# Optimization experiments

Hardware: AMD Instinct MI355X
Metric: run time of the kernel (lower is better)

## Reference

```python
import jax, jax.numpy as jnp
import numpy as np
from jax import lax

B, DIM, H, DM, NH = 32, 16, 128, 256, 8  # batch, in-channels, seq, d_model, n_head


def setup_inputs() -> dict:
    key = jax.random.key(0)
    k1, k2, k3, k4, k5 = jax.random.split(key, 5)
    x = jax.random.normal(k1, (B, DIM, H, DM), jnp.float32)
    conv1_w = jax.random.normal(k2, (3 * NH * DIM, 1, 5, 1), jnp.float32) * 0.1
    conv2_w = jax.random.normal(k3, (3 * NH * DIM, 1, 1, NH), jnp.float32) * 0.1
    w_out_w = jax.random.normal(k4, (DM, DM), jnp.float32) * (1.0 / np.sqrt(DM))
    w_out_b = jax.random.normal(k5, (DM,), jnp.float32) * 0.01
    return dict(x=x, conv1_w=conv1_w, conv2_w=conv2_w, w_out_w=w_out_w, w_out_b=w_out_b)


def reference(x, conv1_w, conv2_w, w_out_w, w_out_b):
    b, dim, h, w = x.shape
    nh = conv2_w.shape[-1]
    dn = ('NCHW', 'OIHW', 'NCHW')
    # grouped conv (5,1), padding 'same' on height, groups=dim
    y = lax.conv_general_dilated(x, conv1_w, (1, 1), [(2, 2), (0, 0)],
                                 dimension_numbers=dn, feature_group_count=dim)
    # depthwise conv (1, nh) stride (1, nh): width w -> w/nh
    y = lax.conv_general_dilated(y, conv2_w, (1, nh), [(0, 0), (0, 0)],
                                 dimension_numbers=dn, feature_group_count=y.shape[1])
    # dropout layers are identity in eval mode
    C = nh * dim
    wp = w // nh
    y = y.reshape(b, 3, C, h, wp)  # 'b (n c) h w -> n b c h w' split, n=3 outer
    q, k, v = y[:, 0], y[:, 1], y[:, 2]  # each [b, C, h, wp]
    scores = jnp.einsum('bcqd,bckd->bcqk', q, k) / jnp.sqrt(jnp.float32(wp))
    attn = jax.nn.softmax(scores, axis=-1)
    o = jnp.einsum('bcqk,bckd->bcqd', attn, v)  # [b, C, h, wp]
    # 'b (c n) h w -> b c h (n w)' with c=dim, n=nh
    o = o.reshape(b, dim, nh, h, wp).transpose(0, 1, 3, 2, 4).reshape(b, dim, h, nh * wp)
    return o @ w_out_w.T + w_out_b
```

## Files before the change

kernel.cpp:

```cpp
#include <hip/hip_runtime.h>
#include <stdint.h>

#define B_   32
#define DIM_ 16
#define H_   128
#define DM_  256
#define NH_  8
#define WP_  32
#define C3_  384

typedef short bf16x8 __attribute__((ext_vector_type(8)));
typedef float f32x4  __attribute__((ext_vector_type(4)));

__device__ __forceinline__ unsigned short f2bfu(float v) {
    unsigned int x = __float_as_uint(v);
    x += 0x7fffu + ((x >> 16) & 1u);
    return (unsigned short)(x >> 16);
}
__device__ __forceinline__ unsigned cvtpk(float lo, float hi) {
    unsigned r;
    asm("v_cvt_pk_bf16_f32 %0, %1, %2" : "=v"(r) : "v"(lo), "v"(hi));
    return r;
}
__device__ __forceinline__ void gl_lds16(const void* g, void* l) {
    __builtin_amdgcn_global_load_lds(
        (const __attribute__((address_space(1))) unsigned int*)g,
        (__attribute__((address_space(3))) unsigned int*)l, 16, 0, 0);
}

__global__ __launch_bounds__(256) void conv_kernel(
    const float* __restrict__ x, const float* __restrict__ w1,
    const float* __restrict__ w2, unsigned short* __restrict__ y2)
{
    __shared__ float wlds[24 * 16];

    const int bid = blockIdx.x;
    const int ht = bid & 1;
    const int g  = (bid >> 1) & 15;
    const int b  = bid >> 5;
    const int tid = threadIdx.x;
    const int wp = tid & 31;
    const int hl = tid >> 5;
    const int h0 = ht * 64 + hl * 8;

    for (int i = tid; i < 384; i += 256) {
        const int oc = i >> 4, ix = i & 15;
        const int o = g * 24 + oc;
        float v = 0.f;
        if (ix < 5)       v = w1[o * 5 + ix];
        else if (ix < 13) v = w2[o * 8 + (ix - 5)];
        wlds[i] = v;
    }

    const float* xbase = x + ((size_t)(b * DIM_ + g) * H_) * DM_ + wp * 8;

    float xr[12][8];
    #pragma unroll
    for (int r = 0; r < 12; ++r) {
        const int hr = h0 - 2 + r;
        if (hr >= 0 && hr < H_) {
            const float4* p = (const float4*)(xbase + (size_t)hr * DM_);
            float4 a = p[0], c = p[1];
            xr[r][0] = a.x; xr[r][1] = a.y; xr[r][2] = a.z; xr[r][3] = a.w;
            xr[r][4] = c.x; xr[r][5] = c.y; xr[r][6] = c.z; xr[r][7] = c.w;
        } else {
            #pragma unroll
            for (int j = 0; j < 8; ++j) xr[r][j] = 0.f;
        }
    }
    __syncthreads();

    unsigned short* yb = y2 + (((size_t)(b * C3_ + g * 24)) * H_ + h0) * WP_ + wp;

    for (int oc = 0; oc < 24; ++oc) {
        const float* wo_ = &wlds[oc * 16];
        float w1r[5], w2r[8];
        {
            float4 a = *(const float4*)(wo_);
            float4 c = *(const float4*)(wo_ + 4);
            float4 d = *(const float4*)(wo_ + 8);
            w1r[0] = a.x; w1r[1] = a.y; w1r[2] = a.z; w1r[3] = a.w;
            w1r[4] = c.x;
            w2r[0] = c.y; w2r[1] = c.z; w2r[2] = c.w;
            w2r[3] = d.x; w2r[4] = d.y; w2r[5] = d.z; w2r[6] = d.w;
            w2r[7] = wo_[12];
        }

        float u[12];
        #pragma unroll
        for (int r = 0; r < 12; ++r) {
            float s = w2r[0] * xr[r][0];
            #pragma unroll
            for (int j = 1; j < 8; ++j) s = fmaf(w2r[j], xr[r][j], s);
            u[r] = s;
        }

        #pragma unroll
        for (int hh = 0; hh < 8; ++hh) {
            float yv = w1r[0] * u[hh];
            #pragma unroll
            for (int t = 1; t < 5; ++t) yv = fmaf(w1r[t], u[hh + t], yv);
            yb[(size_t)oc * (H_ * WP_) + hh * WP_] = f2bfu(yv);
        }
    }
}

__global__ __launch_bounds__(256) void attn_kernel(
    const unsigned short* __restrict__ y2, unsigned short* __restrict__ z)
{
    __shared__ __align__(16) unsigned char sm[40960];

    const int tid = threadIdx.x;
    const int ch = blockIdx.x & 127, b = blockIdx.x >> 7;
    const size_t base = ((size_t)(b * C3_ + ch)) * 4096;
    const uint4* qg = (const uint4*)(y2 + base);
    const uint4* kg = (const uint4*)(y2 + base + 128 * 4096);
    const uint4* vg = (const uint4*)(y2 + base + 256 * 4096);

    #pragma unroll
    for (int r = 0; r < 2; ++r) {
        const int ci  = tid + r * 256;
        const int row = ci >> 2;
        const int c   = ci & 3;
        const int cx  = c ^ ((row >> 1) & 3);
        *(uint4*)(sm + row * 64 + cx * 16)        = qg[ci];
        *(uint4*)(sm + 8192 + row * 64 + cx * 16) = kg[ci];
        uint4 v = vg[ci];
        unsigned short vs[8];
        vs[0] = (unsigned short)(v.x & 0xffffu); vs[1] = (unsigned short)(v.x >> 16);
        vs[2] = (unsigned short)(v.y & 0xffffu); vs[3] = (unsigned short)(v.y >> 16);
        vs[4] = (unsigned short)(v.z & 0xffffu); vs[5] = (unsigned short)(v.z >> 16);
        vs[6] = (unsigned short)(v.w & 0xffffu); vs[7] = (unsigned short)(v.w >> 16);
        const int d0 = c * 8;
        #pragma unroll
        for (int j = 0; j < 8; ++j) {
            const int d = d0 + j;
            *(unsigned short*)(sm + 32768 + d * 256 + ((row * 2) ^ ((d & 7) << 4))) = vs[j];
        }
    }
    __syncthreads();

    const int l  = tid & 63, wv = tid >> 6;
    const int lm = l & 15,  lk = l >> 4;

    bf16x8 qf[2];
    #pragma unroll
    for (int t = 0; t < 2; ++t) {
        const int q = (wv * 2 + t) * 16 + lm;
        qf[t] = *(const bf16x8*)(sm + q * 64 + ((lk ^ ((q >> 1) & 3)) << 4));
    }
    f32x4 acc[8][2];
    #pragma unroll
    for (int rt = 0; rt < 8; ++rt) {
        acc[rt][0] = 0; acc[rt][1] = 0;
    }
    #pragma unroll
    for (int rt = 0; rt < 8; ++rt) {
        const int kr = rt * 16 + lm;
        bf16x8 kf = *(const bf16x8*)(sm + 8192 + kr * 64 + ((lk ^ ((kr >> 1) & 3)) << 4));
        acc[rt][0] = __builtin_amdgcn_mfma_f32_16x16x32_bf16(kf, qf[0], acc[rt][0], 0, 0, 0);
        acc[rt][1] = __builtin_amdgcn_mfma_f32_16x16x32_bf16(kf, qf[1], acc[rt][1], 0, 0, 0);
    }

    const float Cc = 0.17677669529663687f * 1.4426950408889634f;
    float inv[2];
    #pragma unroll
    for (int t = 0; t < 2; ++t) {
        float m = acc[0][t][0];
        #pragma unroll
        for (int rt = 0; rt < 8; ++rt)
            #pragma unroll
            for (int rg = 0; rg < 4; ++rg) m = fmaxf(m, acc[rt][t][rg]);
        m = fmaxf(m, __shfl_xor(m, 16));
        m = fmaxf(m, __shfl_xor(m, 32));
        float s = 0.f;
        #pragma unroll
        for (int rt = 0; rt < 8; ++rt)
            #pragma unroll
            for (int rg = 0; rg < 4; ++rg) {
                float p = exp2f((acc[rt][t][rg] - m) * Cc);
                acc[rt][t][rg] = p; s += p;
            }
        s += __shfl_xor(s, 16);
        s += __shfl_xor(s, 32);
        inv[t] = 1.0f / s;
    }

    __syncthreads();

    #pragma unroll
    for (int t = 0; t < 2; ++t) {
        const int q = (wv * 2 + t) * 16 + lm;
        #pragma unroll
        for (int rt = 0; rt < 8; ++rt) {
            unsigned u0 = cvtpk(acc[rt][t][0] * inv[t], acc[rt][t][1] * inv[t]);
            unsigned u1 = cvtpk(acc[rt][t][2] * inv[t], acc[rt][t][3] * inv[t]);
            const int kb = rt * 32 + lk * 8;
            *(uint2*)(sm + q * 256 + (kb ^ ((q & 7) << 4))) = make_uint2(u0, u1);
        }
    }
    __syncthreads();

    f32x4 o[2][2];
    o[0][0] = 0; o[0][1] = 0; o[1][0] = 0; o[1][1] = 0;
    #pragma unroll
    for (int kc = 0; kc < 4; ++kc) {
        const int cb = kc * 64 + lk * 16;
        bf16x8 av[2], bp[2];
        #pragma unroll
        for (int dt = 0; dt < 2; ++dt) {
            const int d = dt * 16 + lm;
            av[dt] = *(const bf16x8*)(sm + 32768 + d * 256 + (cb ^ ((d & 7) << 4)));
        }
        #pragma unroll
        for (int t = 0; t < 2; ++t) {
            const int q = (wv * 2 + t) * 16 + lm;
            bp[t] = *(const bf16x8*)(sm + q * 256 + (cb ^ ((q & 7) << 4)));
        }
        #pragma unroll
        for (int dt = 0; dt < 2; ++dt)
            #pragma unroll
            for (int t = 0; t < 2; ++t)
                o[dt][t] = __builtin_amdgcn_mfma_f32_16x16x32_bf16(av[dt], bp[t], o[dt][t], 0, 0, 0);
    }

    const int dd = ch >> 3, nn = ch & 7;
    unsigned short* zb = z + ((size_t)(b * DIM_ + dd)) * (H_ * DM_);
    #pragma unroll
    for (int dt = 0; dt < 2; ++dt)
        #pragma unroll
        for (int t = 0; t < 2; ++t) {
            const int q  = (wv * 2 + t) * 16 + lm;
            const int d0 = dt * 16 + lk * 4;
            unsigned u0 = cvtpk(o[dt][t][0], o[dt][t][1]);
            unsigned u1 = cvtpk(o[dt][t][2], o[dt][t][3]);
            *(uint2*)(zb + (size_t)q * DM_ + nn * 32 + d0) = make_uint2(u0, u1);
        }
}

__global__ __launch_bounds__(256) void prep_w(
    const float* __restrict__ w, unsigned short* __restrict__ wh,
    unsigned short* __restrict__ wl)
{
    const int i = blockIdx.x * 1024 + threadIdx.x * 4;
    float4 v = *(const float4*)(w + i);
    float vv[4] = { v.x, v.y, v.z, v.w };
    unsigned short h[4], lo[4];
    #pragma unroll
    for (int j = 0; j < 4; ++j) {
        h[j] = f2bfu(vv[j]);
        float hf = __uint_as_float(((unsigned)h[j]) << 16);
        lo[j] = f2bfu(vv[j] - hf);
    }
    *(uint2*)(wh + i) = make_uint2((unsigned)h[0] | ((unsigned)h[1] << 16),
                                   (unsigned)h[2] | ((unsigned)h[3] << 16));
    *(uint2*)(wl + i) = make_uint2((unsigned)lo[0] | ((unsigned)lo[1] << 16),
                                   (unsigned)lo[2] | ((unsigned)lo[3] << 16));
}

__global__ __launch_bounds__(256) void proj_kernel(
    const unsigned short* __restrict__ zz, const unsigned short* __restrict__ wh,
    const unsigned short* __restrict__ wl, const float* __restrict__ bias,
    float* __restrict__ out)
{
    __shared__ __align__(16) unsigned char sm[65536];
    const int tid = threadIdx.x;
    const int l = tid & 63, wv = tid >> 6, lm = l & 15, lk = l >> 4;
    const unsigned short* zs = zz + (size_t)blockIdx.x * 32768;

    const int g_off = (tid >> 2) * 256 + (tid & 3) * 8;
    const int lds_wv = wv * 1024;

    const int arow0 = wv * 32 + lm;

    f32x4 acc[2][16];
    #pragma unroll
    for (int t = 0; t < 2; ++t)
        #pragma unroll
        for (int nt = 0; nt < 16; ++nt) acc[t][nt] = 0;

    bf16x8 areg[2][2];

    #pragma unroll
    for (int i = 0; i < 8; ++i) {
        const unsigned short* g = (i < 4 ? wh : wl) + g_off + (i & 3) * 16384;
        gl_lds16(g, sm + i * 4096 + lds_wv);
    }
    #pragma unroll
    for (int t = 0; t < 2; ++t)
        areg[0][t] = *(const bf16x8*)(zs + (size_t)(arow0 + t * 16) * 256 + lk * 8);

    __syncthreads();

    #pragma unroll
    for (int kc = 0; kc < 8; ++kc) {
        const int buf = kc & 1;
        if (kc < 7) {
            #pragma unroll
            for (int i = 0; i < 8; ++i) {
                const unsigned short* g = (i < 4 ? wh : wl) + g_off + (i & 3) * 16384 + (kc + 1) * 32;
                gl_lds16(g, sm + (buf ^ 1) * 32768 + i * 4096 + lds_wv);
            }
            #pragma unroll
            for (int t = 0; t < 2; ++t)
                areg[buf ^ 1][t] = *(const bf16x8*)(zs + (size_t)(arow0 + t * 16) * 256 + (kc + 1) * 32 + lk * 8);
        }
        #pragma unroll
        for (int ph = 0; ph < 2; ++ph)
            #pragma unroll
            for (int nt = 0; nt < 16; ++nt) {
                bf16x8 bf = *(const bf16x8*)(sm + buf * 32768 + ph * 16384 + nt * 1024 + lm * 64 + lk * 16);
                acc[0][nt] = __builtin_amdgcn_mfma_f32_16x16x32_bf16(areg[buf][0], bf, acc[0][nt], 0, 0, 0);
                acc[1][nt] = __builtin_amdgcn_mfma_f32_16x16x32_bf16(areg[buf][1], bf, acc[1][nt], 0, 0, 0);
            }
        __syncthreads();
    }

    float* ob = out + (size_t)blockIdx.x * 32768;
    #pragma unroll
    for (int t = 0; t < 2; ++t)
        #pragma unroll
        for (int nt = 0; nt < 16; ++nt) {
            const float bv = bias[nt * 16 + lm];
            #pragma unroll
            for (int rg = 0; rg < 4; ++rg)
                ob[(size_t)(wv * 32 + t * 16 + lk * 4 + rg) * 256 + nt * 16 + lm] = acc[t][nt][rg] + bv;
        }
}

extern "C" void kernel_launch(void* const* d_in, const int* in_sizes, int n_in,
                              void* d_out, int out_size, void* d_ws, size_t ws_size,
                              hipStream_t stream)
{
    const float* x  = (const float*)d_in[0];
    const float* w1 = (const float*)d_in[1];
    const float* w2 = (const float*)d_in[2];
    const float* wo = (const float*)d_in[3];
    const float* wb = (const float*)d_in[4];
    float* out = (float*)d_out;

    unsigned short* y2 = (unsigned short*)d_ws;
    unsigned short* zz = y2 + (size_t)B_ * C3_ * H_ * WP_;
    unsigned short* wh = y2;
    unsigned short* wl = y2 + 65536;

    conv_kernel<<<dim3(1024), dim3(256), 0, stream>>>(x, w1, w2, y2);
    attn_kernel<<<dim3(4096), dim3(256), 0, stream>>>(y2, zz);
    prep_w<<<dim3(64), dim3(256), 0, stream>>>(wo, wh, wl);
    proj_kernel<<<dim3(512), dim3(256), 0, stream>>>(zz, wh, wl, wb, out);
}
```

Baseline: 118.9 us.

## Write V transposed from conv kernel and vectorize conv output stores via LDS

The conv kernel now writes the V channels (o >= 256) directly in a d-major, h-contiguous layout as packed 16-byte stores. Q and K channels are staged through a per-wave LDS tile so each lane emits one 16-byte row store instead of eight scattered 2-byte stores. The attention kernel then copies V into shared memory with single 16-byte writes instead of transposing it element by element. This changes the intermediate buffer layout contract between the two kernels and adds LDS traffic in the conv kernel.

```diff
diff --git a/kernel.cpp b/kernel.cpp
--- a/kernel.cpp
+++ b/kernel.cpp
@@ -33,6 +33,7 @@
     const float* __restrict__ w2, unsigned short* __restrict__ y2)
 {
     __shared__ float wlds[24 * 16];
+    __shared__ __align__(16) unsigned short tlds[4][512];
 
     const int bid = blockIdx.x;
     const int ht = bid & 1;
@@ -42,6 +43,8 @@
     const int wp = tid & 31;
     const int hl = tid >> 5;
     const int h0 = ht * 64 + hl * 8;
+    const int wv = tid >> 6;
+    const int lane = tid & 63;
 
     for (int i = tid; i < 384; i += 256) {
         const int oc = i >> 4, ix = i & 15;
@@ -70,9 +73,11 @@
     }
     __syncthreads();
 
-    unsigned short* yb = y2 + (((size_t)(b * C3_ + g * 24)) * H_ + h0) * WP_ + wp;
+    unsigned char* tw = (unsigned char*)&tlds[wv][0];
+    const int hr_ = lane >> 2, wq_ = lane & 3;
 
     for (int oc = 0; oc < 24; ++oc) {
+        const int o = g * 24 + oc;
         const float* wo_ = &wlds[oc * 16];
         float w1r[5], w2r[8];
         {
@@ -95,12 +100,28 @@
             u[r] = s;
         }
 
+        unsigned short yv[8];
         #pragma unroll
         for (int hh = 0; hh < 8; ++hh) {
-            float yv = w1r[0] * u[hh];
-            #pragma unroll
-            for (int t = 1; t < 5; ++t) yv = fmaf(w1r[t], u[hh + t], yv);
-            yb[(size_t)oc * (H_ * WP_) + hh * WP_] = f2bfu(yv);
+            float y = w1r[0] * u[hh];
+            #pragma unroll
+            for (int t = 1; t < 5; ++t) y = fmaf(w1r[t], u[hh + t], y);
+            yv[hh] = f2bfu(y);
+        }
+
+        if (o >= 256) {
+            uint4 pk;
+            pk.x = (unsigned)yv[0] | ((unsigned)yv[1] << 16);
+            pk.y = (unsigned)yv[2] | ((unsigned)yv[3] << 16);
+            pk.z = (unsigned)yv[4] | ((unsigned)yv[5] << 16);
+            pk.w = (unsigned)yv[6] | ((unsigned)yv[7] << 16);
+            *(uint4*)(y2 + ((size_t)(b * C3_ + o) * 32 + wp) * 128 + h0) = pk;
+        } else {
+            #pragma unroll
+            for (int j = 0; j < 8; ++j)
+                tlds[wv][j * 64 + lane] = yv[j];
+            uint4 vv = *(const uint4*)(tw + (hr_ & 7) * 128 + (hr_ >> 3) * 64 + wq_ * 16);
+            *(uint4*)(y2 + ((size_t)(b * C3_ + o) * 128 + ht * 64 + wv * 16 + hr_) * 32 + wq_ * 8) = vv;
         }
     }
 }
@@ -125,18 +146,9 @@
         const int cx  = c ^ ((row >> 1) & 3);
         *(uint4*)(sm + row * 64 + cx * 16)        = qg[ci];
         *(uint4*)(sm + 8192 + row * 64 + cx * 16) = kg[ci];
-        uint4 v = vg[ci];
-        unsigned short vs[8];
-        vs[0] = (unsigned short)(v.x & 0xffffu); vs[1] = (unsigned short)(v.x >> 16);
-        vs[2] = (unsigned short)(v.y & 0xffffu); vs[3] = (unsigned short)(v.y >> 16);
-        vs[4] = (unsigned short)(v.z & 0xffffu); vs[5] = (unsigned short)(v.z >> 16);
-        vs[6] = (unsigned short)(v.w & 0xffffu); vs[7] = (unsigned short)(v.w >> 16);
-        const int d0 = c * 8;
-        #pragma unroll
-        for (int j = 0; j < 8; ++j) {
-            const int d = d0 + j;
-            *(unsigned short*)(sm + 32768 + d * 256 + ((row * 2) ^ ((d & 7) << 4))) = vs[j];
-        }
+        const int vd = ci >> 4;
+        const int vhc = ci & 15;
+        *(uint4*)(sm + 32768 + vd * 256 + ((vhc * 16) ^ ((vd & 7) << 4))) = vg[ci];
     }
     __syncthreads();
 
```

New measurement: 119.8 us. Within noise of the previous version (+0.8%).
